# Kernel optimization log

Hardware: AMD Instinct MI355X
Metric: run time of the kernel (lower is better)

## Reference

```python
import jax, jax.numpy as jnp
import numpy as np

SCALE = 0.1  # literal .mul(0.1) in the source, not 1/sqrt(d_k)


def setup_inputs() -> dict:
    key = jax.random.key(0)
    kq, kk, kv = jax.random.split(key, 3)
    B, S, D, Dv = 8, 2048, 1024, 1024
    q = jax.random.normal(kq, (B, S, D), dtype=jnp.float32)
    k = jax.random.normal(kk, (B, D, S), dtype=jnp.float32)  # note [B, D, S]: matmul(q, k) with no transpose
    v = jax.random.normal(kv, (B, S, Dv), dtype=jnp.float32)
    return {"q": q, "k": k, "v": v}


def reference(q, k, v):
    # s = (q @ k) * 0.1 ; a = softmax(s, -1) ; dropout in eval -> identity ; r = a @ v
    s = jnp.einsum('bsd,bdt->bst', q, k) * SCALE  # [B, S, S]
    a = jax.nn.softmax(s, axis=-1)
    r = jnp.einsum('bst,btv->bsv', a, v)          # [B, S, Dv]
    return r
```

## Files before the change

### kernel.cpp

```cpp
#include <hip/hip_runtime.h>
#include <stdint.h>

#define SEQ 2048
#define DHK 1024
#define DHV 1024
#define NB 8

typedef __attribute__((ext_vector_type(8))) short bf16x8;
typedef __attribute__((ext_vector_type(4))) float f32x4;
typedef __attribute__((ext_vector_type(4))) uint32_t u32x4;

__device__ __forceinline__ unsigned short f2bf(float f) {
    uint32_t u = __builtin_bit_cast(uint32_t, f);
    u += 0x7fffu + ((u >> 16) & 1u);
    return (unsigned short)(u >> 16);
}

__device__ __forceinline__ uint32_t pack2(float a, float b) {
    return (uint32_t)f2bf(a) | ((uint32_t)f2bf(b) << 16);
}

__device__ __forceinline__ void gload_lds16(const unsigned short* g, unsigned short* l) {
    __builtin_amdgcn_global_load_lds(
        (const __attribute__((address_space(1))) void*)g,
        (__attribute__((address_space(3))) void*)l,
        16, 0, 0);
}

#define WG_BARRIER() asm volatile("s_barrier" ::: "memory")

__global__ __launch_bounds__(256) void fused_cvt(const float* __restrict__ q,
                                                 const float* __restrict__ k,
                                                 const float* __restrict__ v,
                                                 unsigned short* __restrict__ Qb,
                                                 unsigned short* __restrict__ Kt,
                                                 unsigned short* __restrict__ Vt) {
    __shared__ uint32_t t32[64][33];
    int bid = blockIdx.x;
    if (bid < 4096) {
        size_t i = ((size_t)bid * 256 + threadIdx.x) * 16;
#pragma unroll
        for (int hh = 0; hh < 2; ++hh) {
            float4 a = *(const float4*)(q + i + hh * 8);
            float4 b = *(const float4*)(q + i + hh * 8 + 4);
            u32x4 o;
            o.x = pack2(a.x, a.y);
            o.y = pack2(a.z, a.w);
            o.z = pack2(b.x, b.y);
            o.w = pack2(b.z, b.w);
            *(u32x4*)(Qb + i + hh * 8) = o;
        }
        return;
    }
    const float* in;
    unsigned short* out;
    int R, C, b, x, y;
    if (bid < 8192) {
        int id = bid - 4096;
        b = id >> 9; int rem = id & 511;
        x = rem & 31; y = rem >> 5;
        in = k; out = Kt; R = DHK; C = SEQ;
    } else {
        int id = bid - 8192;
        b = id >> 9; int rem = id & 511;
        x = rem & 15; y = rem >> 4;
        in = v; out = Vt; R = SEQ; C = DHV;
    }
    int c0 = x * 64, r0 = y * 64;
    const float* ib = in + (size_t)b * R * C;
    unsigned short* ob = out + (size_t)b * R * C;

    int tr = threadIdx.x >> 4;
    int m  = threadIdx.x & 15;
#pragma unroll
    for (int it = 0; it < 4; ++it) {
        int r = tr + it * 16;
        float4 w = *(const float4*)(ib + (size_t)(r0 + r) * C + c0 + m * 4);
        t32[r][2 * m]     = pack2(w.x, w.y);
        t32[r][2 * m + 1] = pack2(w.z, w.w);
    }
    __syncthreads();

    int cpi = threadIdx.x >> 3;
    int seg = threadIdx.x & 7;
    uint32_t d[8];
#pragma unroll
    for (int j = 0; j < 8; ++j) d[j] = t32[seg * 8 + j][cpi];
    u32x4 lo, hi;
#pragma unroll
    for (int j = 0; j < 4; ++j) {
        lo[j] = (d[2 * j] & 0xFFFFu) | (d[2 * j + 1] << 16);
        hi[j] = (d[2 * j] >> 16) | (d[2 * j + 1] & 0xFFFF0000u);
    }
    int c2 = cpi * 2;
    *(u32x4*)(ob + (size_t)(c0 + c2) * R + r0 + seg * 8) = lo;
    *(u32x4*)(ob + (size_t)(c0 + c2 + 1) * R + r0 + seg * 8) = hi;
}

template <int MODE>
__device__ __forceinline__ void attn_gemm8_body(const unsigned short* __restrict__ A,
                                                const unsigned short* __restrict__ Bt,
                                                void* __restrict__ Cout) {
    constexpr int K  = (MODE == 0) ? DHK : SEQ;
    constexpr int N  = (MODE == 0) ? SEQ : DHV;
    constexpr int TN = N / 256;
    constexpr int NKT = K / 64;
    constexpr int NITER = NKT / 2;

    __shared__ __attribute__((aligned(16))) unsigned short As[2][256 * 64];
    __shared__ __attribute__((aligned(16))) unsigned short Bs[2][256 * 64];

    const int lid   = blockIdx.x;
    const int batch = lid & 7;
    const int t     = lid >> 3;
    const int bm    = t / TN;
    const int bn    = t % TN;

    const int tid  = threadIdx.x;
    const int wv   = tid >> 6;
    const int lane = tid & 63;
    const int wm   = wv & 1;
    const int wn   = wv >> 1;
    const int m16  = lane & 15;
    const int q    = lane >> 4;
    const int sw   = m16 & 7;
    const int lane_row = lane >> 3;
    const int g    = (lane & 7) ^ lane_row;

    const unsigned short* Ab = A  + (size_t)batch * SEQ * K;
    const unsigned short* Bb = Bt + (size_t)batch * N * K;
    const unsigned short* Ag = Ab + (size_t)(bm * 256 + lane_row) * K + g * 8;
    const unsigned short* Bg = Bb + (size_t)(bn * 256 + lane_row) * K + g * 8;

    auto stage = [&](int ktile, int sub) {
        const int buf = ktile & 1;
        const int k0  = ktile * 64;
#pragma unroll
        for (int c = 0; c < 2; ++c) {
            const int lrow = wv * 16 + c * 8;
            if (sub < 2) {
                const int rb = sub * 128 + lrow;
                gload_lds16(Bg + (size_t)rb * K + k0, &Bs[buf][rb * 64]);
            } else {
                const int rb = (sub == 2 ? 0 : 64) + lrow + (lrow & 64);
                gload_lds16(Ag + (size_t)rb * K + k0, &As[buf][rb * 64]);
            }
        }
    };

    f32x4 acc[8][4];
#pragma unroll
    for (int i = 0; i < 8; ++i)
#pragma unroll
        for (int j = 0; j < 4; ++j)
#pragma unroll
            for (int e = 0; e < 4; ++e) acc[i][j][e] = 0.0f;

    f32x4 acc1[8];
#pragma unroll
    for (int i = 0; i < 8; ++i)
#pragma unroll
        for (int e = 0; e < 4; ++e) acc1[i][e] = 0.0f;
    const short one_bf = (short)0x3F80;
    const bf16x8 ones = {one_bf, one_bf, one_bf, one_bf, one_bf, one_bf, one_bf, one_bf};

#pragma unroll
    for (int ht = 0; ht < 7; ++ht) stage(ht >> 2, ht & 3);
    asm volatile("s_waitcnt vmcnt(6)" ::: "memory");
    WG_BARRIER();

    bf16x8 bfr[4][2];
#pragma unroll 1
    for (int it = 0; it < NITER; ++it) {
        const bool notlast = (it + 1 < NITER);
#pragma unroll
        for (int p = 0; p < 8; ++p) {
            const int qd   = p & 3;
            const int rbuf = p >> 2;
            bf16x8 af[2][2];
#pragma unroll
            for (int i = 0; i < 2; ++i) {
                const int mrow = wm * 128 + (qd * 2 + i) * 16 + m16;
#pragma unroll
                for (int ss = 0; ss < 2; ++ss)
                    af[i][ss] = *(const bf16x8*)&As[rbuf][mrow * 64 + ((ss * 4 + q) ^ sw) * 8];
            }
            if (qd == 0) {
#pragma unroll
                for (int nt = 0; nt < 4; ++nt) {
                    const int nrow = wn * 64 + nt * 16 + m16;
#pragma unroll
                    for (int ss = 0; ss < 2; ++ss)
                        bfr[nt][ss] = *(const bf16x8*)&Bs[rbuf][nrow * 64 + ((ss * 4 + q) ^ sw) * 8];
                }
            }
            if (p == 0 || notlast) stage((7 + it * 8 + p) >> 2, (7 + p) & 3);
            WG_BARRIER();
            __builtin_amdgcn_s_setprio(1);
#pragma unroll
            for (int ss = 0; ss < 2; ++ss)
#pragma unroll
                for (int i = 0; i < 2; ++i) {
                    const int mt = qd * 2 + i;
#pragma unroll
                    for (int nt = 0; nt < 4; ++nt)
                        acc[mt][nt] = __builtin_amdgcn_mfma_f32_16x16x32_bf16(
                            af[i][ss], bfr[nt][ss], acc[mt][nt], 0, 0, 0);
                    if (MODE == 1)
                        acc1[mt] = __builtin_amdgcn_mfma_f32_16x16x32_bf16(
                            af[i][ss], ones, acc1[mt], 0, 0, 0);
                }
            __builtin_amdgcn_s_setprio(0);
            if (qd == 3) {
                if (notlast) { asm volatile("s_waitcnt vmcnt(6)" ::: "memory"); }
                else         { asm volatile("s_waitcnt vmcnt(0)" ::: "memory"); }
            }
            WG_BARRIER();
        }
    }

    const int i0 = bm * 256 + wm * 128;
    const int t0 = bn * 256 + wn * 64;
    if (MODE == 0) {
        unsigned short* E = (unsigned short*)Cout + (size_t)batch * SEQ * N;
#pragma unroll
        for (int mt = 0; mt < 8; ++mt)
#pragma unroll
            for (int e = 0; e < 4; ++e) {
                int i = i0 + mt * 16 + q * 4 + e;
#pragma unroll
                for (int nt = 0; nt < 4; ++nt) {
                    int cc = t0 + nt * 16 + m16;
                    E[(size_t)i * N + cc] = f2bf(__expf(0.1f * acc[mt][nt][e]));
                }
            }
    } else {
        float* O = (float*)Cout + (size_t)batch * SEQ * N;
#pragma unroll
        for (int mt = 0; mt < 8; ++mt)
#pragma unroll
            for (int e = 0; e < 4; ++e) {
                int i = i0 + mt * 16 + q * 4 + e;
                float inv = 1.0f / acc1[mt][e];
#pragma unroll
                for (int nt = 0; nt < 4; ++nt) {
                    int cc = t0 + nt * 16 + m16;
                    O[(size_t)i * N + cc] = acc[mt][nt][e] * inv;
                }
            }
    }
}

__global__ __launch_bounds__(512, 2) void attn_gemm8_qk(const unsigned short* __restrict__ A,
                                                        const unsigned short* __restrict__ Bt,
                                                        void* __restrict__ Cout) {
    attn_gemm8_body<0>(A, Bt, Cout);
}

__global__ __launch_bounds__(512, 2) void attn_gemm8_pv(const unsigned short* __restrict__ A,
                                                        const unsigned short* __restrict__ Bt,
                                                        void* __restrict__ Cout) {
    attn_gemm8_body<1>(A, Bt, Cout);
}

extern "C" void kernel_launch(void* const* d_in, const int* in_sizes, int n_in,
                              void* d_out, int out_size, void* d_ws, size_t ws_size,
                              hipStream_t stream) {
    (void)in_sizes; (void)n_in; (void)out_size; (void)ws_size;
    const float* q = (const float*)d_in[0];
    const float* k = (const float*)d_in[1];
    const float* v = (const float*)d_in[2];

    char* ws = (char*)d_ws;
    unsigned short* Qb = (unsigned short*)(ws);
    unsigned short* Kt = (unsigned short*)(ws + 33554432);
    unsigned short* Vt = (unsigned short*)(ws + 67108864);
    unsigned short* E  = (unsigned short*)(ws + 100663296);

    fused_cvt<<<dim3(12288), dim3(256), 0, stream>>>(q, k, v, Qb, Kt, Vt);
    attn_gemm8_qk<<<dim3(NB * 8 * 8), dim3(512), 0, stream>>>(Qb, Kt, (void*)E);
    attn_gemm8_pv<<<dim3(NB * 8 * 4), dim3(512), 0, stream>>>(E, Vt, d_out);
}
```

Measured before the change: 364.5 us.

## Fuse QK and PV GEMMs into one cooperative kernel with grid sync

Replaces the two separate GEMM launches with a single cooperative kernel of 256 blocks. Each block computes two QK tiles, then a grid-wide barrier runs before each block computes one PV tile. This removes one kernel launch and the gap between the two phases. In exchange, the QK phase now runs 256 persistent blocks doing two tiles each instead of 512 blocks, and the grid sync adds its own cost; the tail behaviour is unclear.

```diff
diff --git a/kernel.cpp b/kernel.cpp
--- a/kernel.cpp
+++ b/kernel.cpp
@@ -1,4 +1,5 @@
 #include <hip/hip_runtime.h>
+#include <hip/hip_cooperative_groups.h>
 #include <stdint.h>
 
 #define SEQ 2048
@@ -98,19 +99,16 @@
 }
 
 template <int MODE>
-__device__ __forceinline__ void attn_gemm8_body(const unsigned short* __restrict__ A,
-                                                const unsigned short* __restrict__ Bt,
-                                                void* __restrict__ Cout) {
+__device__ __forceinline__ void gemm_body(const unsigned short* __restrict__ A,
+                                          const unsigned short* __restrict__ Bt,
+                                          void* __restrict__ Cout, int lid,
+                                          unsigned short* AsB, unsigned short* BsB) {
     constexpr int K  = (MODE == 0) ? DHK : SEQ;
     constexpr int N  = (MODE == 0) ? SEQ : DHV;
     constexpr int TN = N / 256;
     constexpr int NKT = K / 64;
     constexpr int NITER = NKT / 2;
 
-    __shared__ __attribute__((aligned(16))) unsigned short As[2][256 * 64];
-    __shared__ __attribute__((aligned(16))) unsigned short Bs[2][256 * 64];
-
-    const int lid   = blockIdx.x;
     const int batch = lid & 7;
     const int t     = lid >> 3;
     const int bm    = t / TN;
@@ -140,10 +138,10 @@
             const int lrow = wv * 16 + c * 8;
             if (sub < 2) {
                 const int rb = sub * 128 + lrow;
-                gload_lds16(Bg + (size_t)rb * K + k0, &Bs[buf][rb * 64]);
+                gload_lds16(Bg + (size_t)rb * K + k0, BsB + buf * 16384 + rb * 64);
             } else {
                 const int rb = (sub == 2 ? 0 : 64) + lrow + (lrow & 64);
-                gload_lds16(Ag + (size_t)rb * K + k0, &As[buf][rb * 64]);
+                gload_lds16(Ag + (size_t)rb * K + k0, AsB + buf * 16384 + rb * 64);
             }
         }
     };
@@ -183,7 +181,7 @@
                 const int mrow = wm * 128 + (qd * 2 + i) * 16 + m16;
 #pragma unroll
                 for (int ss = 0; ss < 2; ++ss)
-                    af[i][ss] = *(const bf16x8*)&As[rbuf][mrow * 64 + ((ss * 4 + q) ^ sw) * 8];
+                    af[i][ss] = *(const bf16x8*)(AsB + rbuf * 16384 + mrow * 64 + ((ss * 4 + q) ^ sw) * 8);
             }
             if (qd == 0) {
 #pragma unroll
@@ -191,7 +189,7 @@
                     const int nrow = wn * 64 + nt * 16 + m16;
 #pragma unroll
                     for (int ss = 0; ss < 2; ++ss)
-                        bfr[nt][ss] = *(const bf16x8*)&Bs[rbuf][nrow * 64 + ((ss * 4 + q) ^ sw) * 8];
+                        bfr[nt][ss] = *(const bf16x8*)(BsB + rbuf * 16384 + nrow * 64 + ((ss * 4 + q) ^ sw) * 8);
                 }
             }
             if (p == 0 || notlast) stage((7 + it * 8 + p) >> 2, (7 + p) & 3);
@@ -251,16 +249,21 @@
     }
 }
 
-__global__ __launch_bounds__(512, 2) void attn_gemm8_qk(const unsigned short* __restrict__ A,
-                                                        const unsigned short* __restrict__ Bt,
-                                                        void* __restrict__ Cout) {
-    attn_gemm8_body<0>(A, Bt, Cout);
-}
-
-__global__ __launch_bounds__(512, 2) void attn_gemm8_pv(const unsigned short* __restrict__ A,
-                                                        const unsigned short* __restrict__ Bt,
-                                                        void* __restrict__ Cout) {
-    attn_gemm8_body<1>(A, Bt, Cout);
+__global__ __launch_bounds__(512, 2) void attn_qkpv(const unsigned short* __restrict__ Qb,
+                                                    const unsigned short* __restrict__ Kt,
+                                                    const unsigned short* __restrict__ Vt,
+                                                    unsigned short* __restrict__ E,
+                                                    float* __restrict__ Out) {
+    __shared__ __attribute__((aligned(16))) unsigned short As[2 * 16384];
+    __shared__ __attribute__((aligned(16))) unsigned short Bs[2 * 16384];
+
+    gemm_body<0>(Qb, Kt, (void*)E, blockIdx.x, As, Bs);
+    gemm_body<0>(Qb, Kt, (void*)E, blockIdx.x + 256, As, Bs);
+
+    __threadfence();
+    cooperative_groups::this_grid().sync();
+
+    gemm_body<1>(E, Vt, (void*)Out, blockIdx.x, As, Bs);
 }
 
 extern "C" void kernel_launch(void* const* d_in, const int* in_sizes, int n_in,
@@ -276,8 +279,11 @@
     unsigned short* Kt = (unsigned short*)(ws + 33554432);
     unsigned short* Vt = (unsigned short*)(ws + 67108864);
     unsigned short* E  = (unsigned short*)(ws + 100663296);
+    float* Outp = (float*)d_out;
 
     fused_cvt<<<dim3(12288), dim3(256), 0, stream>>>(q, k, v, Qb, Kt, Vt);
-    attn_gemm8_qk<<<dim3(NB * 8 * 8), dim3(512), 0, stream>>>(Qb, Kt, (void*)E);
-    attn_gemm8_pv<<<dim3(NB * 8 * 4), dim3(512), 0, stream>>>(E, Vt, d_out);
-}
+
+    void* args[] = {(void*)&Qb, (void*)&Kt, (void*)&Vt, (void*)&E, (void*)&Outp};
+    hipLaunchCooperativeKernel((const void*)attn_qkpv, dim3(256), dim3(512),
+                               args, 0, stream);
+}
```

Result: slower. 497.8 us (+36.6%).
